# Optimization experiments

Measured on AMD Instinct MI355X. Metric: run time of the kernel, lower is better.

Reference implementation:

```python
import jax, jax.numpy as jnp
import numpy as np

N_NODES = 50000
K_NEIGH = 32
D_IN = 128
D_OUT = 128
LEAKY_ALPHA = 0.2  # tf.nn.leaky_relu default


def setup_inputs() -> dict:
    key = jax.random.key(0)
    k1, k2, k3, k4 = jax.random.split(key, 4)
    glorot = lambda k, shape: jax.random.uniform(
        k, shape, jnp.float32, -1.0, 1.0) * np.sqrt(6.0 / (shape[0] + shape[1]))
    return {
        "self_vecs": jax.random.normal(k1, (N_NODES, D_IN), jnp.float32),
        "neigh_vecs": jax.random.normal(k2, (N_NODES * K_NEIGH, D_IN), jnp.float32),
        "feat_weights": glorot(k3, (D_IN, D_OUT)),
        "attn_weights": glorot(k4, (D_OUT, 1)),
        "bias": jnp.zeros((D_OUT,), jnp.float32),
        "num_neighbors": K_NEIGH,
    }


def reference(self_vecs, neigh_vecs, feat_weights, attn_weights, bias, num_neighbors):
    n = self_vecs.shape[0]
    from_neighs = neigh_vecs @ feat_weights            # [N*K, Dout]
    h_self = self_vecs @ feat_weights                  # [N, Dout]
    neigh_logits = (from_neighs @ attn_weights).reshape(n, num_neighbors)  # [N, K]
    self_logits = h_self @ attn_weights                # [N, 1]
    logits = neigh_logits + self_logits                # [N, K]
    coefs = jax.nn.softmax(jax.nn.leaky_relu(logits, LEAKY_ALPHA), axis=-1)
    # dropout rate = 0.0 -> identity
    h_neighs = jnp.einsum("nk,nkd->nd", coefs,
                          from_neighs.reshape(n, num_neighbors, -1))  # [N, Dout]
    return jax.nn.relu(h_self + h_neighs + bias)
```

## Files before the change

kernel.cpp:

```cpp
#include <hip/hip_runtime.h>


constexpr int D   = 128;
constexpr int KN  = 32;
constexpr int NPB = 8;
constexpr int XS_ROWS = 48;
constexpr int LDP = 136;

typedef __bf16 bf16;
typedef __attribute__((ext_vector_type(8))) __bf16 bf16x8;
typedef __attribute__((ext_vector_type(4))) __bf16 bf16x4;
typedef __attribute__((ext_vector_type(4))) float  f32x4;

__global__ void prep_wt_kernel(const float* __restrict__ W, bf16* __restrict__ Wt) {
  int i = blockIdx.x * 256 + threadIdx.x;
  if (i < D * D) {
    int n = i >> 7, k = i & 127;
    Wt[i] = (bf16)W[(k << 7) + n];
  }
}

__global__ __launch_bounds__(256, 3)
void gat_kernel(const float* __restrict__ selfv,
                const float* __restrict__ neighv,
                const float* __restrict__ Wfp,
                const bf16*  __restrict__ Wt_g,
                const float* __restrict__ attn,
                const float* __restrict__ biasp,
                float* __restrict__ out,
                int nnodes, int use_ws)
{
  __shared__ __align__(16) bf16 Wt[D][LDP];
  __shared__ __align__(16) bf16 Xs[XS_ROWS][LDP];
  __shared__ float lp[4][KN];
  __shared__ float slp[4];
  __shared__ float coefs[KN];

  const int tid  = threadIdx.x;
  const int w    = tid >> 6;
  const int lane = tid & 63;
  const int q    = lane >> 4;
  const int l15  = lane & 15;
  const int colbase = w << 5;

  if (use_ws) {
    const ulonglong2* src = (const ulonglong2*)Wt_g;
    for (int i = tid; i < (D * D) / 8; i += 256) {
      int r = i >> 4, c8 = i & 15;
      *(ulonglong2*)&Wt[r][c8 << 3] = src[i];
    }
  } else {
    for (int i = tid; i < D * D; i += 256) {
      int n = i >> 7, k = i & 127;
      Wt[n][k] = (bf16)Wfp[(k << 7) + n];
    }
  }
  for (int i = tid; i < (XS_ROWS - 33) * LDP; i += 256)
    (&Xs[33][0])[i] = (bf16)0.0f;

  const float a0 = attn[colbase + l15];
  const float a1 = attn[colbase + 16 + l15];
  const float b0 = biasp[colbase + l15];
  const float b1 = biasp[colbase + 16 + l15];

  __syncthreads();

  bf16x8 Bf[2][4];
  #pragma unroll
  for (int nt = 0; nt < 2; ++nt)
    #pragma unroll
    for (int ks = 0; ks < 4; ++ks)
      Bf[nt][ks] = *(const bf16x8*)&Wt[colbase + nt * 16 + l15][ks * 32 + q * 8];

  const int node0 = blockIdx.x * NPB;
  const float4* neigh4 = (const float4*)neighv;
  const float4* self4  = (const float4*)selfv;

  float4 pn[4];
  float4 ps;

  auto load_node = [&](int node) {
    size_t base = (size_t)node * (KN * D / 4);
    #pragma unroll
    for (int i = 0; i < 4; ++i) pn[i] = neigh4[base + tid + i * 256];
    if (tid < 32) ps = self4[(size_t)node * (D / 4) + tid];
  };
  auto store_node_lds = [&]() {
    #pragma unroll
    for (int i = 0; i < 4; ++i) {
      int idx4 = tid + i * 256;
      int row = idx4 >> 5, c4 = idx4 & 31;
      bf16x4 v = { (bf16)pn[i].x, (bf16)pn[i].y, (bf16)pn[i].z, (bf16)pn[i].w };
      *(bf16x4*)&Xs[row][c4 << 2] = v;
    }
    if (tid < 32) {
      bf16x4 v = { (bf16)ps.x, (bf16)ps.y, (bf16)ps.z, (bf16)ps.w };
      *(bf16x4*)&Xs[32][tid << 2] = v;
    }
  };

  if (node0 < nnodes) { load_node(node0); store_node_lds(); }

  for (int ni = 0; ni < NPB; ++ni) {
    const int node = node0 + ni;
    const bool valid = node < nnodes;
    __syncthreads();

    const bool pvalid = (ni + 1 < NPB) && (node + 1 < nnodes);
    if (pvalid) load_node(node + 1);

    f32x4 acc[3][2];
    if (valid) {
      #pragma unroll
      for (int mt = 0; mt < 3; ++mt)
        #pragma unroll
        for (int nt = 0; nt < 2; ++nt)
          acc[mt][nt] = (f32x4){0.f, 0.f, 0.f, 0.f};

      #pragma unroll
      for (int ks = 0; ks < 4; ++ks) {
        bf16x8 Af[3];
        #pragma unroll
        for (int mt = 0; mt < 3; ++mt)
          Af[mt] = *(const bf16x8*)&Xs[mt * 16 + l15][ks * 32 + q * 8];
        #pragma unroll
        for (int mt = 0; mt < 3; ++mt)
          #pragma unroll
          for (int nt = 0; nt < 2; ++nt)
            acc[mt][nt] = __builtin_amdgcn_mfma_f32_16x16x32_bf16(
                Af[mt], Bf[nt][ks], acc[mt][nt], 0, 0, 0);
      }

      #pragma unroll
      for (int mt = 0; mt < 2; ++mt) {
        #pragma unroll
        for (int r = 0; r < 4; ++r) {
          float v = acc[mt][0][r] * a0 + acc[mt][1][r] * a1;
          v += __shfl_xor(v, 1); v += __shfl_xor(v, 2);
          v += __shfl_xor(v, 4); v += __shfl_xor(v, 8);
          if (l15 == 0) lp[w][mt * 16 + (q << 2) + r] = v;
        }
      }
      {
        float v = acc[2][0][0] * a0 + acc[2][1][0] * a1;
        v += __shfl_xor(v, 1); v += __shfl_xor(v, 2);
        v += __shfl_xor(v, 4); v += __shfl_xor(v, 8);
        if (lane == 0) slp[w] = v;
      }
    }
    __syncthreads();

    if (valid && w == 0) {
      float sl = slp[0] + slp[1] + slp[2] + slp[3];
      float t = 0.f;
      if (lane < 32) t = lp[0][lane] + lp[1][lane] + lp[2][lane] + lp[3][lane] + sl;
      t = t > 0.f ? t : 0.2f * t;
      float m = t;
      #pragma unroll
      for (int msk = 16; msk >= 1; msk >>= 1) m = fmaxf(m, __shfl_xor(m, msk, 32));
      float e = __expf(t - m);
      float s = e;
      #pragma unroll
      for (int msk = 16; msk >= 1; msk >>= 1) s += __shfl_xor(s, msk, 32);
      if (lane < 32) coefs[lane] = e / s;
    }
    __syncthreads();

    if (valid) {
      #pragma unroll
      for (int nt = 0; nt < 2; ++nt) {
        float p = 0.f;
        #pragma unroll
        for (int mt = 0; mt < 2; ++mt)
          #pragma unroll
          for (int r = 0; r < 4; ++r)
            p += coefs[mt * 16 + (q << 2) + r] * acc[mt][nt][r];
        p += __shfl_xor(p, 16);
        p += __shfl_xor(p, 32);
        float ov = acc[2][nt][0] + p + (nt ? b1 : b0);
        ov = fmaxf(ov, 0.f);
        if (lane < 16) out[(size_t)node * D + colbase + nt * 16 + lane] = ov;
      }
    }
    __syncthreads();
    if (pvalid) store_node_lds();
  }
}

extern "C" void kernel_launch(void* const* d_in, const int* in_sizes, int n_in,
                              void* d_out, int out_size, void* d_ws, size_t ws_size,
                              hipStream_t stream) {
  const float* selfv  = (const float*)d_in[0];
  const float* neighv = (const float*)d_in[1];
  const float* W      = (const float*)d_in[2];
  const float* attn   = (const float*)d_in[3];
  const float* biasp  = (const float*)d_in[4];
  float* out = (float*)d_out;
  const int nnodes = in_sizes[0] / D;

  const int use_ws = (ws_size >= (size_t)(D * D * sizeof(bf16))) ? 1 : 0;
  bf16* Wt_g = (bf16*)d_ws;
  if (use_ws)
    prep_wt_kernel<<<(D * D + 255) / 256, 256, 0, stream>>>(W, Wt_g);

  const int nblocks = (nnodes + NPB - 1) / NPB;
  gat_kernel<<<nblocks, 256, 0, stream>>>(selfv, neighv, W, Wt_g, attn, biasp,
                                          out, nnodes, use_ws);
}
```

Before: 1.101 ms.

## Assign one node per wavefront and drop block-wide barriers from the GAT kernel

Each wavefront now processes its own nodes end to end. It computes all 128 output columns with MFMA, reading the weight fragments from LDS every k-step. The softmax and the weighted neighbour sum stay in registers via lane shuffles, so the four `__syncthreads` per node and the LDS staging of logits and coefficients are gone. The goal is to remove cross-wave synchronisation stalls and put more neighbour bytes in flight per CU. In exchange, accumulator register use grows, launch bounds drop to 2 blocks per CU, and the previous register prefetch of the next node is removed. Padding-row reads for the third M-tile now overlap other waves' LDS regions or uninitialised memory.

```diff
diff --git a/kernel.cpp b/kernel.cpp
--- a/kernel.cpp
+++ b/kernel.cpp
@@ -3,9 +3,10 @@
 
 constexpr int D   = 128;
 constexpr int KN  = 32;
-constexpr int NPB = 8;
-constexpr int XS_ROWS = 48;
+constexpr int NPW = 4;
 constexpr int LDP = 136;
+constexpr int XR  = 33;
+constexpr int XROWS_TOTAL = 4 * XR + 15;
 
 typedef __bf16 bf16;
 typedef __attribute__((ext_vector_type(8))) __bf16 bf16x8;
@@ -20,7 +21,7 @@
   }
 }
 
-__global__ __launch_bounds__(256, 3)
+__global__ __launch_bounds__(256, 2)
 void gat_kernel(const float* __restrict__ selfv,
                 const float* __restrict__ neighv,
                 const float* __restrict__ Wfp,
@@ -31,17 +32,13 @@
                 int nnodes, int use_ws)
 {
   __shared__ __align__(16) bf16 Wt[D][LDP];
-  __shared__ __align__(16) bf16 Xs[XS_ROWS][LDP];
-  __shared__ float lp[4][KN];
-  __shared__ float slp[4];
-  __shared__ float coefs[KN];
+  __shared__ __align__(16) bf16 Xs[XROWS_TOTAL][LDP];
 
   const int tid  = threadIdx.x;
   const int w    = tid >> 6;
   const int lane = tid & 63;
   const int q    = lane >> 4;
   const int l15  = lane & 15;
-  const int colbase = w << 5;
 
   if (use_ws) {
     const ulonglong2* src = (const ulonglong2*)Wt_g;
@@ -55,135 +52,127 @@
       Wt[n][k] = (bf16)Wfp[(k << 7) + n];
     }
   }
-  for (int i = tid; i < (XS_ROWS - 33) * LDP; i += 256)
-    (&Xs[33][0])[i] = (bf16)0.0f;
 
-  const float a0 = attn[colbase + l15];
-  const float a1 = attn[colbase + 16 + l15];
-  const float b0 = biasp[colbase + l15];
-  const float b1 = biasp[colbase + 16 + l15];
+  float av[8], bv[8];
+  #pragma unroll
+  for (int nt = 0; nt < 8; ++nt) {
+    av[nt] = attn[nt * 16 + l15];
+    bv[nt] = biasp[nt * 16 + l15];
+  }
 
   __syncthreads();
 
-  bf16x8 Bf[2][4];
-  #pragma unroll
-  for (int nt = 0; nt < 2; ++nt)
-    #pragma unroll
-    for (int ks = 0; ks < 4; ++ks)
-      Bf[nt][ks] = *(const bf16x8*)&Wt[colbase + nt * 16 + l15][ks * 32 + q * 8];
-
-  const int node0 = blockIdx.x * NPB;
+  bf16* Xw = &Xs[w * XR][0];
   const float4* neigh4 = (const float4*)neighv;
   const float4* self4  = (const float4*)selfv;
+  const int gw = blockIdx.x * 4 + w;
 
-  float4 pn[4];
-  float4 ps;
+  for (int i = 0; i < NPW; ++i) {
+    const int node = gw * NPW + i;
+    if (node >= nnodes) break;
 
-  auto load_node = [&](int node) {
-    size_t base = (size_t)node * (KN * D / 4);
+    {
+      const size_t nb = (size_t)node * (KN * D / 4);
+      const size_t sb = (size_t)node * (D / 4);
+      #pragma unroll
+      for (int it = 0; it < 17; ++it) {
+        int idx = lane + it * 64;
+        if (idx < 1056) {
+          float4 v = (idx < 1024) ? neigh4[nb + idx] : self4[sb + (idx - 1024)];
+          int row = idx >> 5, c4 = idx & 31;
+          bf16x4 b = { (bf16)v.x, (bf16)v.y, (bf16)v.z, (bf16)v.w };
+          *(bf16x4*)&Xw[row * LDP + (c4 << 2)] = b;
+        }
+      }
+    }
+    __threadfence_block();
+
+    f32x4 acc[3][8];
     #pragma unroll
-    for (int i = 0; i < 4; ++i) pn[i] = neigh4[base + tid + i * 256];
-    if (tid < 32) ps = self4[(size_t)node * (D / 4) + tid];
-  };
-  auto store_node_lds = [&]() {
+    for (int mt = 0; mt < 3; ++mt)
+      #pragma unroll
+      for (int nt = 0; nt < 8; ++nt)
+        acc[mt][nt] = (f32x4){0.f, 0.f, 0.f, 0.f};
+
     #pragma unroll
-    for (int i = 0; i < 4; ++i) {
-      int idx4 = tid + i * 256;
-      int row = idx4 >> 5, c4 = idx4 & 31;
-      bf16x4 v = { (bf16)pn[i].x, (bf16)pn[i].y, (bf16)pn[i].z, (bf16)pn[i].w };
-      *(bf16x4*)&Xs[row][c4 << 2] = v;
-    }
-    if (tid < 32) {
-      bf16x4 v = { (bf16)ps.x, (bf16)ps.y, (bf16)ps.z, (bf16)ps.w };
-      *(bf16x4*)&Xs[32][tid << 2] = v;
-    }
-  };
-
-  if (node0 < nnodes) { load_node(node0); store_node_lds(); }
-
-  for (int ni = 0; ni < NPB; ++ni) {
-    const int node = node0 + ni;
-    const bool valid = node < nnodes;
-    __syncthreads();
-
-    const bool pvalid = (ni + 1 < NPB) && (node + 1 < nnodes);
-    if (pvalid) load_node(node + 1);
-
-    f32x4 acc[3][2];
-    if (valid) {
+    for (int ks = 0; ks < 4; ++ks) {
+      bf16x8 A[3], B[8];
+      #pragma unroll
+      for (int mt = 0; mt < 3; ++mt)
+        A[mt] = *(const bf16x8*)&Xw[(mt * 16 + l15) * LDP + ks * 32 + q * 8];
+      #pragma unroll
+      for (int nt = 0; nt < 8; ++nt)
+        B[nt] = *(const bf16x8*)&Wt[nt * 16 + l15][ks * 32 + q * 8];
       #pragma unroll
       for (int mt = 0; mt < 3; ++mt)
         #pragma unroll
-        for (int nt = 0; nt < 2; ++nt)
-          acc[mt][nt] = (f32x4){0.f, 0.f, 0.f, 0.f};
+        for (int nt = 0; nt < 8; ++nt)
+          acc[mt][nt] = __builtin_amdgcn_mfma_f32_16x16x32_bf16(A[mt], B[nt], acc[mt][nt], 0, 0, 0);
+    }
 
+    float lg[2][4];
+    #pragma unroll
+    for (int mt = 0; mt < 2; ++mt)
       #pragma unroll
-      for (int ks = 0; ks < 4; ++ks) {
-        bf16x8 Af[3];
+      for (int r = 0; r < 4; ++r) {
+        float v = 0.f;
         #pragma unroll
-        for (int mt = 0; mt < 3; ++mt)
-          Af[mt] = *(const bf16x8*)&Xs[mt * 16 + l15][ks * 32 + q * 8];
-        #pragma unroll
-        for (int mt = 0; mt < 3; ++mt)
-          #pragma unroll
-          for (int nt = 0; nt < 2; ++nt)
-            acc[mt][nt] = __builtin_amdgcn_mfma_f32_16x16x32_bf16(
-                Af[mt], Bf[nt][ks], acc[mt][nt], 0, 0, 0);
-      }
-
-      #pragma unroll
-      for (int mt = 0; mt < 2; ++mt) {
-        #pragma unroll
-        for (int r = 0; r < 4; ++r) {
-          float v = acc[mt][0][r] * a0 + acc[mt][1][r] * a1;
-          v += __shfl_xor(v, 1); v += __shfl_xor(v, 2);
-          v += __shfl_xor(v, 4); v += __shfl_xor(v, 8);
-          if (l15 == 0) lp[w][mt * 16 + (q << 2) + r] = v;
-        }
-      }
-      {
-        float v = acc[2][0][0] * a0 + acc[2][1][0] * a1;
+        for (int nt = 0; nt < 8; ++nt) v += acc[mt][nt][r] * av[nt];
         v += __shfl_xor(v, 1); v += __shfl_xor(v, 2);
         v += __shfl_xor(v, 4); v += __shfl_xor(v, 8);
-        if (lane == 0) slp[w] = v;
+        lg[mt][r] = v;
       }
+    float sl;
+    {
+      float v = 0.f;
+      #pragma unroll
+      for (int nt = 0; nt < 8; ++nt) v += acc[2][nt][0] * av[nt];
+      v += __shfl_xor(v, 1); v += __shfl_xor(v, 2);
+      v += __shfl_xor(v, 4); v += __shfl_xor(v, 8);
+      sl = __shfl(v, l15);
     }
-    __syncthreads();
 
-    if (valid && w == 0) {
-      float sl = slp[0] + slp[1] + slp[2] + slp[3];
-      float t = 0.f;
-      if (lane < 32) t = lp[0][lane] + lp[1][lane] + lp[2][lane] + lp[3][lane] + sl;
-      t = t > 0.f ? t : 0.2f * t;
-      float m = t;
+    float e[2][4];
+    float mx = -3.4e38f;
+    #pragma unroll
+    for (int mt = 0; mt < 2; ++mt)
       #pragma unroll
-      for (int msk = 16; msk >= 1; msk >>= 1) m = fmaxf(m, __shfl_xor(m, msk, 32));
-      float e = __expf(t - m);
-      float s = e;
+      for (int r = 0; r < 4; ++r) {
+        float t = lg[mt][r] + sl;
+        t = t > 0.f ? t : 0.2f * t;
+        e[mt][r] = t;
+        mx = fmaxf(mx, t);
+      }
+    mx = fmaxf(mx, __shfl_xor(mx, 16));
+    mx = fmaxf(mx, __shfl_xor(mx, 32));
+    float s = 0.f;
+    #pragma unroll
+    for (int mt = 0; mt < 2; ++mt)
       #pragma unroll
-      for (int msk = 16; msk >= 1; msk >>= 1) s += __shfl_xor(s, msk, 32);
-      if (lane < 32) coefs[lane] = e / s;
+      for (int r = 0; r < 4; ++r) {
+        e[mt][r] = __expf(e[mt][r] - mx);
+        s += e[mt][r];
+      }
+    s += __shfl_xor(s, 16);
+    s += __shfl_xor(s, 32);
+    const float inv = 1.0f / s;
+
+    #pragma unroll
+    for (int nt = 0; nt < 8; ++nt) {
+      float p = 0.f;
+      #pragma unroll
+      for (int mt = 0; mt < 2; ++mt)
+        #pragma unroll
+        for (int r = 0; r < 4; ++r)
+          p += e[mt][r] * acc[mt][nt][r];
+      p *= inv;
+      p += __shfl_xor(p, 16);
+      p += __shfl_xor(p, 32);
+      float hs = __shfl(acc[2][nt][0], l15);
+      float ov = fmaxf(hs + p + bv[nt], 0.f);
+      if (q == (nt >> 1))
+        out[(size_t)node * D + nt * 16 + l15] = ov;
     }
-    __syncthreads();
-
-    if (valid) {
-      #pragma unroll
-      for (int nt = 0; nt < 2; ++nt) {
-        float p = 0.f;
-        #pragma unroll
-        for (int mt = 0; mt < 2; ++mt)
-          #pragma unroll
-          for (int r = 0; r < 4; ++r)
-            p += coefs[mt * 16 + (q << 2) + r] * acc[mt][nt][r];
-        p += __shfl_xor(p, 16);
-        p += __shfl_xor(p, 32);
-        float ov = acc[2][nt][0] + p + (nt ? b1 : b0);
-        ov = fmaxf(ov, 0.f);
-        if (lane < 16) out[(size_t)node * D + colbase + nt * 16 + lane] = ov;
-      }
-    }
-    __syncthreads();
-    if (pvalid) store_node_lds();
   }
 }
 
@@ -203,7 +192,8 @@
   if (use_ws)
     prep_wt_kernel<<<(D * D + 255) / 256, 256, 0, stream>>>(W, Wt_g);
 
-  const int nblocks = (nnodes + NPB - 1) / NPB;
+  const int nwaves  = (nnodes + NPW - 1) / NPW;
+  const int nblocks = (nwaves + 3) / 4;
   gat_kernel<<<nblocks, 256, 0, stream>>>(selfv, neighv, W, Wt_g, attn, biasp,
                                           out, nnodes, use_ws);
 }
```

New measurement: 1.078 ms. 2.2% less time.
